# Kernel tuning notes

Hardware: AMD Instinct MI355X
Metric: run time of the kernel (lower is better)

## Reference

```python
import jax, jax.numpy as jnp
import numpy as np

B, V, M, H, L, T = 4, 2048, 8192, 64, 5, 4


def setup_inputs() -> dict:
    key = jax.random.key(0)
    ks = jax.random.split(key, 24)
    inp = {
        "input_llr": jax.random.normal(ks[0], (B, V), jnp.float32),
        "message_to_var_mapping": jax.random.randint(ks[1], (M,), 0, V, jnp.int32),
        "message_types": jax.random.randint(ks[2], (M,), 0, T, jnp.int32),
        "var_to_check_adjacency": jax.random.uniform(ks[3], (M, M), jnp.float32),
        "check_to_var_adjacency": jax.random.uniform(ks[4], (M, M), jnp.float32),
    }
    s = 0.05
    # input_embedding: Linear(1, H)
    inp["w_in"] = jax.random.normal(ks[5], (H,), jnp.float32) * s
    inp["b_in"] = jax.random.normal(ks[6], (H,), jnp.float32) * s
    # per-layer params, stacked over L iterations
    inp["type_emb"] = jax.random.normal(ks[7], (L, T, H), jnp.float32) * s
    inp["w1v"] = jax.random.normal(ks[8], (L, 2 * H, H), jnp.float32) * s
    inp["b1v"] = jax.random.normal(ks[9], (L, H), jnp.float32) * s
    inp["w2v"] = jax.random.normal(ks[10], (L, H, H), jnp.float32) * s
    inp["b2v"] = jax.random.normal(ks[11], (L, H), jnp.float32) * s
    inp["w1c"] = jax.random.normal(ks[12], (L, 2 * H, H), jnp.float32) * s
    inp["b1c"] = jax.random.normal(ks[13], (L, H), jnp.float32) * s
    inp["w2c"] = jax.random.normal(ks[14], (L, H, H), jnp.float32) * s
    inp["b2c"] = jax.random.normal(ks[15], (L, H), jnp.float32) * s
    # output_projection of the LAST gnn layer (the one used by decode_messages)
    inp["proj_w"] = jax.random.normal(ks[16], (H,), jnp.float32) * s
    inp["proj_b"] = jax.random.normal(ks[17], (), jnp.float32) * s
    return inp


def reference(input_llr, message_to_var_mapping, message_types,
              var_to_check_adjacency, check_to_var_adjacency,
              w_in, b_in, type_emb, w1v, b1v, w2v, b2v,
              w1c, b1c, w2c, b2c, proj_w, proj_b):
    Bv, Vn = input_llr.shape
    # gather message LLRs from variable nodes: (B, M)
    msg_llr = input_llr[:, message_to_var_mapping]
    # input embedding Linear(1, H): (B, M, H)
    feat = msg_llr[..., None] * w_in + b_in
    safe_types = jnp.clip(message_types, 0, T - 1)
    n_layers = type_emb.shape[0]
    for i in range(n_layers):
        te = type_emb[i][safe_types]                      # (M, H)
        comb = feat + te                                  # (B, M, H)
        v2c = jnp.einsum('mn,bnh->bmh', var_to_check_adjacency, comb)
        uv = jnp.concatenate([comb, v2c], axis=-1)        # (B, M, 2H)
        uv = jax.nn.relu(uv @ w1v[i] + b1v[i]) @ w2v[i] + b2v[i]
        c2v = jnp.einsum('mn,bnh->bmh', check_to_var_adjacency, comb)
        uc = jnp.concatenate([comb, c2v], axis=-1)
        uc = jax.nn.relu(uc @ w1c[i] + b1c[i]) @ w2c[i] + b2c[i]
        upd = uv + uc
        if i > 0:  # residual applied only after first iteration (per source)
            upd = upd + feat
        feat = upd
    # decode with last layer's output projection: (B, M)
    decoded = feat @ proj_w + proj_b
    # sum-aggregate message LLRs back to variable nodes: (B, V)
    var_llrs = jax.ops.segment_sum(decoded.T, message_to_var_mapping,
                                   num_segments=Vn).T
    return jax.nn.sigmoid(var_llrs + input_llr)
```

## Files before the change

kernel.cpp:

```cpp
#include <hip/hip_runtime.h>
#include <math.h>

static constexpr int CB = 4;
static constexpr int CV = 2048;
static constexpr int CM = 8192;
static constexpr int CH = 64;
static constexpr int CL = 5;
static constexpr int CT = 4;
static constexpr int RR = CM * CB;
static constexpr int WCAT_STRIDE = 192 * 128 + 128 * 64 + 128 + 64;
static constexpr size_t SLAB = (size_t)CM * 256;

typedef float f32x4 __attribute__((ext_vector_type(4)));
typedef short bf16x8 __attribute__((ext_vector_type(8)));
typedef unsigned int u32;
typedef unsigned short u16;

__device__ inline u16 f2bf(float x) {
    u32 u = __float_as_uint(x);
    u += 0x7FFF + ((u >> 16) & 1);
    return (u16)(u >> 16);
}
__device__ inline float bf2f(u16 b) { return __uint_as_float(((u32)b) << 16); }

#define GLOAD16(gp, lp)                                                         \
    __builtin_amdgcn_global_load_lds(                                           \
        (const __attribute__((address_space(1))) unsigned int*)(gp),            \
        (__attribute__((address_space(3))) unsigned int*)(lp), 16, 0, 0)

__global__ void k_init_feat(const float* __restrict__ llr, const int* __restrict__ map,
                            const float* __restrict__ w_in, const float* __restrict__ b_in,
                            float* __restrict__ feat) {
    int idx = blockIdx.x * blockDim.x + threadIdx.x;
    int h = idx & 63;
    int r = idx >> 6;
    int m = r >> 2;
    int b = r & 3;
    float v = llr[b * CV + map[m]];
    feat[idx] = v * w_in[h] + b_in[h];
}

__global__ void k_comb(const float* __restrict__ feat, const int* __restrict__ types,
                       const float* __restrict__ te, float* __restrict__ in2) {
    int idx = blockIdx.x * blockDim.x + threadIdx.x;
    int h = idx & 63;
    int r = idx >> 6;
    int m = r >> 2;
    int t = types[m];
    t = t < 0 ? 0 : (t > CT - 1 ? CT - 1 : t);
    in2[(size_t)r * 192 + h] = feat[idx] + te[t * CH + h];
}

__global__ __launch_bounds__(256) void k_splitA(const float* __restrict__ Avc,
                                                const float* __restrict__ Acv,
                                                u16* __restrict__ Aprep) {
    __shared__ float lds[16][548];
    const int blk = blockIdx.x;
    const int adj = blk >> 13;
    const int rem = blk & 8191;
    const int rf = rem & 511;
    const int kig = rem >> 9;
    const float* __restrict__ A = adj ? Acv : Avc;
    const int t = threadIdx.x;
    {
        const int rl = t >> 4, cc = t & 15;
        const float* rp = A + (size_t)(rf * 16 + rl) * CM + kig * 512 + cc * 32;
        const int cbase = cc * 32 + ((cc & 7) << 2);
#pragma unroll
        for (int j = 0; j < 8; ++j) {
            float4 v = *(const float4*)(rp + j * 4);
            *(float4*)&lds[rl][cbase + j * 4] = v;
        }
    }
    __syncthreads();
    {
        const int lane = t & 63, w = t >> 6;
        const int r = lane & 15, c = lane >> 4;
#pragma unroll
        for (int i = 0; i < 4; ++i) {
            const int kl = w * 4 + i;
            const int cbase = kl * 32 + ((kl & 7) << 2) + c * 8;
            float4 v0 = *(const float4*)&lds[r][cbase];
            float4 v1 = *(const float4*)&lds[r][cbase + 4];
            float e[8] = {v0.x, v0.y, v0.z, v0.w, v1.x, v1.y, v1.z, v1.w};
            u32 hw[4], lw[4];
#pragma unroll
            for (int j = 0; j < 4; ++j) {
                float a0 = e[2 * j], a1 = e[2 * j + 1];
                u16 h0 = f2bf(a0), h1 = f2bf(a1);
                u16 g0 = f2bf(a0 - bf2f(h0)), g1 = f2bf(a1 - bf2f(h1));
                hw[j] = (u32)h0 | ((u32)h1 << 16);
                lw[j] = (u32)g0 | ((u32)g1 << 16);
            }
            u16* dp = Aprep + (((size_t)adj * 256 + kig * 16 + kl) * 512 + rf) * 1024
                    + (size_t)lane * 8;
            *(uint4*)dp = make_uint4(hw[0], hw[1], hw[2], hw[3]);
            *(uint4*)(dp + 512) = make_uint4(lw[0], lw[1], lw[2], lw[3]);
        }
    }
}

__global__ void k_transposeB(const float* __restrict__ feat, const int* __restrict__ types,
                             const float* __restrict__ te, char* __restrict__ BprepC,
                             float* __restrict__ comb) {
    __shared__ float tile[64][65];
    __shared__ float teL[4][64];
    __shared__ int ty[64];
    const int tid = threadIdx.x;
    const int m0 = blockIdx.x * 64;
    teL[tid >> 6][tid & 63] = te[tid];
    if (tid < 64) {
        int tt = types[m0 + tid];
        ty[tid] = tt < 0 ? 0 : (tt > CT - 1 ? CT - 1 : tt);
    }
    __syncthreads();
    for (int b = 0; b < 4; ++b) {
        __syncthreads();
        {
            const int mr = tid >> 2, hc = (tid & 3) * 16;
            const float* fp = feat + ((size_t)(m0 + mr) * 4 + b) * 64 + hc;
            float* op = comb + ((size_t)(m0 + mr) * 4 + b) * 64 + hc;
            const int tt = ty[mr];
#pragma unroll
            for (int j = 0; j < 4; ++j) {
                float4 v = *(const float4*)(fp + j * 4);
                float4 c;
                c.x = v.x + teL[tt][hc + j * 4 + 0];
                c.y = v.y + teL[tt][hc + j * 4 + 1];
                c.z = v.z + teL[tt][hc + j * 4 + 2];
                c.w = v.w + teL[tt][hc + j * 4 + 3];
                tile[mr][hc + j * 4 + 0] = c.x;
                tile[mr][hc + j * 4 + 1] = c.y;
                tile[mr][hc + j * 4 + 2] = c.z;
                tile[mr][hc + j * 4 + 3] = c.w;
                *(float4*)(op + j * 4) = c;
            }
        }
        __syncthreads();
        {
            const int h = tid & 63, mg = tid >> 6;
            u32 hw[8], lw[8];
#pragma unroll
            for (int q = 0; q < 8; ++q) {
                float v0 = tile[mg * 16 + 2 * q + 0][h];
                float v1 = tile[mg * 16 + 2 * q + 1][h];
                u16 h0 = f2bf(v0), h1 = f2bf(v1);
                u16 g0 = f2bf(v0 - bf2f(h0)), g1 = f2bf(v1 - bf2f(h1));
                hw[q] = (u32)h0 | ((u32)h1 << 16);
                lw[q] = (u32)g0 | ((u32)g1 << 16);
            }
            const int c = b * 64 + h;
            const int mstart = m0 + mg * 16;
            const int ki = mstart >> 5;
            const int q0 = (mstart >> 3) & 3;
            const int swzc = (c & 7) << 4;
            char* rowp = BprepC + (size_t)ki * 32768 + c * 128;
            *(uint4*)(rowp + (((q0 + 0) * 16) ^ swzc)) = make_uint4(hw[0], hw[1], hw[2], hw[3]);
            *(uint4*)(rowp + (((q0 + 1) * 16) ^ swzc)) = make_uint4(hw[4], hw[5], hw[6], hw[7]);
            *(uint4*)(rowp + (((4 + q0) * 16) ^ swzc)) = make_uint4(lw[0], lw[1], lw[2], lw[3]);
            *(uint4*)(rowp + (((5 + q0) * 16) ^ swzc)) = make_uint4(lw[4], lw[5], lw[6], lw[7]);
        }
    }
}

__global__ __launch_bounds__(512, 1) void k_adjmfma_fast(
    const char* __restrict__ AprepC, const char* __restrict__ BprepC,
    float* __restrict__ pbuf) {
    __shared__ char frames[3][49152];

    int lin = blockIdx.y * 64 + blockIdx.x;
    lin = (lin & 7) * 32 + (lin >> 3);
    const int bx = lin & 63;
    const int by = lin >> 6;
    const int adj = by >> 1;
    const int ks = by & 1;

    const int tid = threadIdx.x;
    const int lane = tid & 63;
    const int wid = tid >> 6;
    const int wr = wid >> 2;
    const int wc = wid & 3;
    const int l15 = lane & 15, l4 = lane >> 4;
    const int m0 = bx * 128;

    const size_t abase = (((size_t)adj * 256) * 512 + (size_t)bx * 8) * 2048;

#define STAGE3(FP, S)                                                            \
    {                                                                            \
        int ki_ = ks * 128 + (S); if (ki_ > 255) ki_ = 255;                      \
        const char* as_ = AprepC + abase + (size_t)ki_ * (512 * 2048);           \
        GLOAD16(as_ + tid * 16, (FP) + tid * 16);                                \
        GLOAD16(as_ + 8192 + tid * 16, (FP) + 8192 + tid * 16);                  \
        const char* bs_ = BprepC + ((size_t)ki_ << 15);                          \
        GLOAD16(bs_ + tid * 16, (FP) + 16384 + tid * 16);                        \
        GLOAD16(bs_ + 8192 + tid * 16, (FP) + 24576 + tid * 16);                 \
        GLOAD16(bs_ + 16384 + tid * 16, (FP) + 32768 + tid * 16);                \
        GLOAD16(bs_ + 24576 + tid * 16, (FP) + 40960 + tid * 16);                \
    }

    f32x4 acc[4][4] = {};

    STAGE3(&frames[0][0], 0);
    STAGE3(&frames[1][0], 1);
    STAGE3(&frames[2][0], 2);

    int f = 0;
    for (int s = 0; s < 128; ++s) {
        asm volatile("s_waitcnt vmcnt(12)" ::: "memory");
        asm volatile("s_barrier" ::: "memory");
        const char* fr = &frames[f][0];
        bf16x8 bh[4], bl[4];
#pragma unroll
        for (int nf = 0; nf < 4; ++nf) {
            const int col = wc * 64 + nf * 16 + l15;
            const char* rb = fr + 16384 + col * 128;
            const int swz = (col & 7) << 4;
            bh[nf] = *(const bf16x8*)(rb + ((l4 * 16) ^ swz));
            bl[nf] = *(const bf16x8*)(rb + (((4 + l4) * 16) ^ swz));
        }
#pragma unroll
        for (int mf = 0; mf < 4; ++mf) {
            const char* ra = fr + (wr * 4 + mf) * 2048 + lane * 16;
            bf16x8 ah = *(const bf16x8*)ra;
            bf16x8 al = *(const bf16x8*)(ra + 1024);
#pragma unroll
            for (int nf = 0; nf < 4; ++nf) {
                acc[mf][nf] = __builtin_amdgcn_mfma_f32_16x16x32_bf16(ah, bh[nf], acc[mf][nf], 0, 0, 0);
                acc[mf][nf] = __builtin_amdgcn_mfma_f32_16x16x32_bf16(ah, bl[nf], acc[mf][nf], 0, 0, 0);
                acc[mf][nf] = __builtin_amdgcn_mfma_f32_16x16x32_bf16(al, bh[nf], acc[mf][nf], 0, 0, 0);
            }
        }
        asm volatile("s_barrier" ::: "memory");
        STAGE3(fr, s + 3);
        f = (f == 2) ? 0 : f + 1;
    }
    asm volatile("s_waitcnt vmcnt(0)" ::: "memory");

    float* pb = pbuf + (size_t)by * SLAB;
#pragma unroll
    for (int mf = 0; mf < 4; ++mf) {
#pragma unroll
        for (int nf = 0; nf < 4; ++nf) {
            const int col = wc * 64 + nf * 16 + l15;
#pragma unroll
            for (int r = 0; r < 4; ++r) {
                const int m = m0 + wr * 64 + mf * 16 + l4 * 4 + r;
                pb[(size_t)m * 256 + col] = acc[mf][nf][r];
            }
        }
    }
#undef STAGE3
}

__global__ __launch_bounds__(256) void k_gemm1f(
    const float* __restrict__ comb, const float* __restrict__ pbuf,
    const float* __restrict__ wc, float* __restrict__ hid) {
    __shared__ float As[32][64];
    __shared__ float Bs[32][68];

    const int tid = threadIdx.x;
    const int m0 = blockIdx.y * 64;
    const int c0 = blockIdx.x * 64;
    const int tm = (tid & 15) * 4;
    const int tn = (tid >> 4) * 4;
    const int arow = tid & 63;
    const int akg = (tid >> 6) * 8;
    const int bk = tid >> 4;
    const int bc = (tid & 15) * 4;
    const float* bias = wc + 32768;

    float acc[4][4] = {};

    for (int k0 = 0; k0 < 192; k0 += 32) {
        const int krow = k0 + akg;
        const int r = m0 + arow;
        float4 a0, a1;
        if (krow < 64) {
            const float* ap = comb + (size_t)r * 64 + krow;
            a0 = *(const float4*)ap;
            a1 = *(const float4*)(ap + 4);
        } else {
            const int adj = (krow - 64) >> 6;
            const int h = (krow - 64) & 63;
            const float* p = pbuf + (size_t)(adj * 2) * SLAB
                           + (size_t)(r >> 2) * 256 + (r & 3) * 64 + h;
            float4 x0 = *(const float4*)p;
            float4 x1 = *(const float4*)(p + 4);
            float4 y0 = *(const float4*)(p + SLAB);
            float4 y1 = *(const float4*)(p + SLAB + 4);
            a0.x = x0.x + y0.x; a0.y = x0.y + y0.y; a0.z = x0.z + y0.z; a0.w = x0.w + y0.w;
            a1.x = x1.x + y1.x; a1.y = x1.y + y1.y; a1.z = x1.z + y1.z; a1.w = x1.w + y1.w;
        }
        float4 b0 = *(const float4*)(wc + (size_t)(k0 + bk) * 128 + c0 + bc);
        float4 b1 = *(const float4*)(wc + (size_t)(k0 + bk + 16) * 128 + c0 + bc);
        As[akg + 0][arow] = a0.x;
        As[akg + 1][arow] = a0.y;
        As[akg + 2][arow] = a0.z;
        As[akg + 3][arow] = a0.w;
        As[akg + 4][arow] = a1.x;
        As[akg + 5][arow] = a1.y;
        As[akg + 6][arow] = a1.z;
        As[akg + 7][arow] = a1.w;
        *(float4*)&Bs[bk][bc] = b0;
        *(float4*)&Bs[bk + 16][bc] = b1;
        __syncthreads();
#pragma unroll
        for (int k = 0; k < 32; ++k) {
            float4 av = *(const float4*)&As[k][tm];
            float4 bv = *(const float4*)&Bs[k][tn];
            float a_[4] = {av.x, av.y, av.z, av.w};
            float b_[4] = {bv.x, bv.y, bv.z, bv.w};
#pragma unroll
            for (int i = 0; i < 4; ++i)
#pragma unroll
                for (int j = 0; j < 4; ++j)
                    acc[i][j] = fmaf(a_[i], b_[j], acc[i][j]);
        }
        __syncthreads();
    }

#pragma unroll
    for (int i = 0; i < 4; ++i) {
        int m = m0 + tm + i;
        float4 x = make_float4(acc[i][0], acc[i][1], acc[i][2], acc[i][3]);
        const float4 bv = *(const float4*)&bias[c0 + tn];
        x.x = fmaxf(x.x + bv.x, 0.f);
        x.y = fmaxf(x.y + bv.y, 0.f);
        x.z = fmaxf(x.z + bv.z, 0.f);
        x.w = fmaxf(x.w + bv.w, 0.f);
        *(float4*)&hid[(size_t)m * 128 + c0 + tn] = x;
    }
}

__global__ void k_transpose(const float* __restrict__ feat, const int* __restrict__ types,
                            const float* __restrict__ te,
                            u16* __restrict__ BH, u16* __restrict__ BL) {
    __shared__ float tile[64][65];
    __shared__ float teL[4][64];
    __shared__ int ty[64];
    const int tid = threadIdx.x;
    const int m0 = blockIdx.x * 64;
    teL[tid >> 6][tid & 63] = te[tid];
    if (tid < 64) {
        int t = types[m0 + tid];
        ty[tid] = t < 0 ? 0 : (t > CT - 1 ? CT - 1 : t);
    }
    __syncthreads();
    for (int b = 0; b < 4; ++b) {
        __syncthreads();
        {
            const int mr = tid >> 2, hc = (tid & 3) * 16;
            const float* fp = feat + ((size_t)(m0 + mr) * 4 + b) * 64 + hc;
            const int t = ty[mr];
#pragma unroll
            for (int j = 0; j < 4; ++j) {
                float4 v = *(const float4*)(fp + j * 4);
                tile[mr][hc + j * 4 + 0] = v.x + teL[t][hc + j * 4 + 0];
                tile[mr][hc + j * 4 + 1] = v.y + teL[t][hc + j * 4 + 1];
                tile[mr][hc + j * 4 + 2] = v.z + teL[t][hc + j * 4 + 2];
                tile[mr][hc + j * 4 + 3] = v.w + teL[t][hc + j * 4 + 3];
            }
        }
        __syncthreads();
        {
            const int h = tid & 63, mg = tid >> 6;
            u32 hw[8], lw[8];
#pragma unroll
            for (int q = 0; q < 8; ++q) {
                float v0 = tile[mg * 16 + 2 * q + 0][h];
                float v1 = tile[mg * 16 + 2 * q + 1][h];
                u16 h0 = f2bf(v0), h1 = f2bf(v1);
                u16 g0 = f2bf(v0 - bf2f(h0)), g1 = f2bf(v1 - bf2f(h1));
                hw[q] = (u32)h0 | ((u32)h1 << 16);
                lw[q] = (u32)g0 | ((u32)g1 << 16);
            }
            size_t obase = (size_t)(b * 64 + h) * CM + m0 + mg * 16;
            *(uint4*)(BH + obase) = make_uint4(hw[0], hw[1], hw[2], hw[3]);
            *(uint4*)(BH + obase + 8) = make_uint4(hw[4], hw[5], hw[6], hw[7]);
            *(uint4*)(BL + obase) = make_uint4(lw[0], lw[1], lw[2], lw[3]);
            *(uint4*)(BL + obase + 8) = make_uint4(lw[4], lw[5], lw[6], lw[7]);
        }
    }
}

__global__ __launch_bounds__(512, 2) void k_adjmfma_fb(
    const float* __restrict__ A0, const float* __restrict__ A1,
    const u16* __restrict__ BH, const u16* __restrict__ BL,
    float* __restrict__ pbuf) {
    __shared__ char lA[128 * 128];
    __shared__ char lB[256 * 128];

    const int tid = threadIdx.x;
    const int adj = blockIdx.y >> 1;
    const int ks = blockIdx.y & 1;
    const int m0 = blockIdx.x * 128;
    const float* __restrict__ A = adj ? A1 : A0;
    const int kbase = ks * 4096;

    const int lane = tid & 63;
    const int wid = tid >> 6;
    const int wr = wid >> 2;
    const int wc = wid & 3;
    const int l15 = lane & 15, l4 = lane >> 4;

    const int sa_row = tid >> 2, sa_kq = tid & 3;
    const int sb_col = tid >> 1, sb_part = tid & 1;

    f32x4 acc[4][4] = {};

    for (int k0 = 0; k0 < 4096; k0 += 32) {
        {
            const float* ap = A + (size_t)(m0 + sa_row) * CM + kbase + k0 + sa_kq * 8;
            float4 v0 = *(const float4*)ap;
            float4 v1 = *(const float4*)(ap + 4);
            float vv[8] = {v0.x, v0.y, v0.z, v0.w, v1.x, v1.y, v1.z, v1.w};
            u32 hw[4], lw[4];
#pragma unroll
            for (int j = 0; j < 4; ++j) {
                float a0 = vv[2 * j], a1 = vv[2 * j + 1];
                u16 h0 = f2bf(a0), h1 = f2bf(a1);
                u16 g0 = f2bf(a0 - bf2f(h0)), g1 = f2bf(a1 - bf2f(h1));
                hw[j] = (u32)h0 | ((u32)h1 << 16);
                lw[j] = (u32)g0 | ((u32)g1 << 16);
            }
            char* base = lA + sa_row * 128;
            const int swz = (sa_row & 7) << 4;
            *(uint4*)(base + ((sa_kq * 16) ^ swz)) = make_uint4(hw[0], hw[1], hw[2], hw[3]);
            *(uint4*)(base + ((64 + sa_kq * 16) ^ swz)) = make_uint4(lw[0], lw[1], lw[2], lw[3]);
        }
        {
            const u16* src = (sb_part ? BL : BH) + (size_t)sb_col * CM + kbase + k0;
            char* base = lB + sb_col * 128;
            const int swz = (sb_col & 7) << 4;
            const int lb = sb_part * 64;
#pragma unroll
            for (int j = 0; j < 4; ++j) {
                uint4 v = *(const uint4*)(src + j * 8);
                *(uint4*)(base + ((lb + j * 16) ^ swz)) = v;
            }
        }
        __syncthreads();

        bf16x8 bh[4], bl[4];
#pragma unroll
        for (int nf = 0; nf < 4; ++nf) {
            const int col = wc * 64 + nf * 16 + l15;
            const char* rb = lB + col * 128;
            const int swz = (col & 7) << 4;
            bh[nf] = *(const bf16x8*)(rb + ((l4 * 16) ^ swz));
            bl[nf] = *(const bf16x8*)(rb + ((64 + l4 * 16) ^ swz));
        }
#pragma unroll
        for (int mf = 0; mf < 4; ++mf) {
            const int row = wr * 64 + mf * 16 + l15;
            const char* ra = lA + row * 128;
            const int swz = (row & 7) << 4;
            bf16x8 ah = *(const bf16x8*)(ra + ((l4 * 16) ^ swz));
            bf16x8 al = *(const bf16x8*)(ra + ((64 + l4 * 16) ^ swz));
#pragma unroll
            for (int nf = 0; nf < 4; ++nf) {
                acc[mf][nf] = __builtin_amdgcn_mfma_f32_16x16x32_bf16(ah, bh[nf], acc[mf][nf], 0, 0, 0);
                acc[mf][nf] = __builtin_amdgcn_mfma_f32_16x16x32_bf16(ah, bl[nf], acc[mf][nf], 0, 0, 0);
                acc[mf][nf] = __builtin_amdgcn_mfma_f32_16x16x32_bf16(al, bh[nf], acc[mf][nf], 0, 0, 0);
            }
        }
        __syncthreads();
    }

    float* pb = pbuf + (size_t)blockIdx.y * SLAB;
#pragma unroll
    for (int mf = 0; mf < 4; ++mf) {
#pragma unroll
        for (int nf = 0; nf < 4; ++nf) {
            const int col = wc * 64 + nf * 16 + l15;
#pragma unroll
            for (int r = 0; r < 4; ++r) {
                const int m = m0 + wr * 64 + mf * 16 + l4 * 4 + r;
                pb[(size_t)m * 256 + col] = acc[mf][nf][r];
            }
        }
    }
}

__global__ void k_reduce(const float* __restrict__ pbuf, float* __restrict__ in2) {
    int idx = blockIdx.x * blockDim.x + threadIdx.x;
    int adj = idx >> 19;
    int rem = idx & ((1 << 19) - 1);
    int m = rem >> 6;
    int f4 = rem & 63;
    size_t o = (size_t)m * 256 + (size_t)f4 * 4;
    const float* p0 = pbuf + (size_t)(adj * 2) * SLAB;
    const float* p1 = p0 + SLAB;
    float4 a = *(const float4*)(p0 + o);
    float4 b4 = *(const float4*)(p1 + o);
    a.x += b4.x; a.y += b4.y; a.z += b4.z; a.w += b4.w;
    int col = f4 * 4;
    int bb = col >> 6, h = col & 63;
    *(float4*)&in2[((size_t)m * 4 + bb) * 192 + 64 + adj * 64 + h] = a;
}

__global__ void k_prep(const float* __restrict__ w1v, const float* __restrict__ b1v,
                       const float* __restrict__ w2v, const float* __restrict__ b2v,
                       const float* __restrict__ w1c, const float* __restrict__ b1c,
                       const float* __restrict__ w2c, const float* __restrict__ b2c,
                       float* __restrict__ wcat) {
    int idx = blockIdx.x * blockDim.x + threadIdx.x;
    int total = CL * WCAT_STRIDE;
    if (idx >= total) return;
    int i = idx / WCAT_STRIDE;
    int e = idx % WCAT_STRIDE;
    float v;
    if (e < 24576) {
        int j = e >> 7, k = e & 127;
        if (j < 64)        v = (k < 64) ? w1v[(i * 128 + j) * 64 + k]
                                        : w1c[(i * 128 + j) * 64 + (k - 64)];
        else if (j < 128)  v = (k < 64) ? w1v[(i * 128 + j) * 64 + k] : 0.f;
        else               v = (k < 64) ? 0.f : w1c[(i * 128 + (j - 64)) * 64 + (k - 64)];
    } else if (e < 32768) {
        int e2 = e - 24576; int k = e2 >> 6, h = e2 & 63;
        v = (k < 64) ? w2v[(i * 64 + k) * 64 + h]
                     : w2c[(i * 64 + (k - 64)) * 64 + h];
    } else if (e < 32896) {
        int k = e - 32768;
        v = (k < 64) ? b1v[i * 64 + k] : b1c[i * 64 + (k - 64)];
    } else {
        int h = e - 32896;
        v = b2v[i * 64 + h] + b2c[i * 64 + h];
    }
    wcat[idx] = v;
}

template<int OMODE, int RES>
__global__ __launch_bounds__(256) void k_gemm(
    const float* __restrict__ A0, int lda,
    const float* __restrict__ Bm, int ldb,
    float* __restrict__ O, const float* __restrict__ bias,
    const float* __restrict__ resid, int K) {
    __shared__ float As[32][64];
    __shared__ float Bs[32][68];

    const int tid = threadIdx.x;
    const int m0 = blockIdx.y * 64;
    const int c0 = blockIdx.x * 64;
    const int tm = (tid & 15) * 4;
    const int tn = (tid >> 4) * 4;
    const int arow = tid & 63;
    const int akg = (tid >> 6) * 8;
    const int bk = tid >> 4;
    const int bc = (tid & 15) * 4;

    float acc[4][4] = {};

    for (int k0 = 0; k0 < K; k0 += 32) {
        const float* Ap = A0 + (size_t)(m0 + arow) * (size_t)lda + k0 + akg;
        float4 a0 = *(const float4*)Ap;
        float4 a1 = *(const float4*)(Ap + 4);
        float4 b0 = *(const float4*)(Bm + (size_t)(k0 + bk) * (size_t)ldb + c0 + bc);
        float4 b1 = *(const float4*)(Bm + (size_t)(k0 + bk + 16) * (size_t)ldb + c0 + bc);
        As[akg + 0][arow] = a0.x;
        As[akg + 1][arow] = a0.y;
        As[akg + 2][arow] = a0.z;
        As[akg + 3][arow] = a0.w;
        As[akg + 4][arow] = a1.x;
        As[akg + 5][arow] = a1.y;
        As[akg + 6][arow] = a1.z;
        As[akg + 7][arow] = a1.w;
        *(float4*)&Bs[bk][bc] = b0;
        *(float4*)&Bs[bk + 16][bc] = b1;
        __syncthreads();
#pragma unroll
        for (int k = 0; k < 32; ++k) {
            float4 av = *(const float4*)&As[k][tm];
            float4 bv = *(const float4*)&Bs[k][tn];
            float a_[4] = {av.x, av.y, av.z, av.w};
            float b_[4] = {bv.x, bv.y, bv.z, bv.w};
#pragma unroll
            for (int i = 0; i < 4; ++i)
#pragma unroll
                for (int j = 0; j < 4; ++j)
                    acc[i][j] = fmaf(a_[i], b_[j], acc[i][j]);
        }
        __syncthreads();
    }

#pragma unroll
    for (int i = 0; i < 4; ++i) {
        int m = m0 + tm + i;
        float4 x = make_float4(acc[i][0], acc[i][1], acc[i][2], acc[i][3]);
        if (OMODE == 1) {
            const float4 bv = *(const float4*)&bias[c0 + tn];
            x.x = fmaxf(x.x + bv.x, 0.f);
            x.y = fmaxf(x.y + bv.y, 0.f);
            x.z = fmaxf(x.z + bv.z, 0.f);
            x.w = fmaxf(x.w + bv.w, 0.f);
            *(float4*)&O[(size_t)m * 128 + c0 + tn] = x;
        } else {
            const float4 bv = *(const float4*)&bias[tn];
            x.x += bv.x; x.y += bv.y; x.z += bv.z; x.w += bv.w;
            if (RES) {
                const float4 rv = *(const float4*)&resid[(size_t)m * 64 + tn];
                x.x += rv.x; x.y += rv.y; x.z += rv.z; x.w += rv.w;
            }
            *(float4*)&O[(size_t)m * 64 + tn] = x;
        }
    }
}

__global__ void k_zero(float* __restrict__ p, int n) {
    int i = blockIdx.x * blockDim.x + threadIdx.x;
    if (i < n) p[i] = 0.f;
}

__global__ void k_decode(const float* __restrict__ feat, const float* __restrict__ proj_w,
                         const float* __restrict__ proj_b, const int* __restrict__ map,
                         float* __restrict__ var_llrs) {
    int r = blockIdx.x * 4 + (threadIdx.x >> 6);
    int lane = threadIdx.x & 63;
    float v = feat[(size_t)r * 64 + lane] * proj_w[lane];
#pragma unroll
    for (int off = 32; off > 0; off >>= 1) v += __shfl_down(v, off);
    if (lane == 0) {
        int m = r >> 2, b = r & 3;
        atomicAdd(&var_llrs[b * CV + map[m]], v + proj_b[0]);
    }
}

__global__ void k_final(const float* __restrict__ var_llrs, const float* __restrict__ llr,
                        float* __restrict__ out) {
    int i = blockIdx.x * blockDim.x + threadIdx.x;
    float x = var_llrs[i] + llr[i];
    out[i] = 1.f / (1.f + expf(-x));
}

extern "C" void kernel_launch(void* const* d_in, const int* in_sizes, int n_in,
                              void* d_out, int out_size, void* d_ws, size_t ws_size,
                              hipStream_t stream) {
    const float* llr   = (const float*)d_in[0];
    const int*   map   = (const int*)d_in[1];
    const int*   types = (const int*)d_in[2];
    const float* Avc   = (const float*)d_in[3];
    const float* Acv   = (const float*)d_in[4];
    const float* w_in  = (const float*)d_in[5];
    const float* b_in  = (const float*)d_in[6];
    const float* temb  = (const float*)d_in[7];
    const float* w1v   = (const float*)d_in[8];
    const float* b1v   = (const float*)d_in[9];
    const float* w2v   = (const float*)d_in[10];
    const float* b2v   = (const float*)d_in[11];
    const float* w1c   = (const float*)d_in[12];
    const float* b1c   = (const float*)d_in[13];
    const float* w2c   = (const float*)d_in[14];
    const float* b2c   = (const float*)d_in[15];
    const float* projw = (const float*)d_in[16];
    const float* projb = (const float*)d_in[17];
    float* out = (float*)d_out;

    constexpr size_t OFF_FEAT = 0;
    constexpr size_t OFF_IN2  = OFF_FEAT + (size_t)RR * 64 * 4;
    constexpr size_t OFF_HID  = OFF_IN2 + (size_t)RR * 192 * 4;
    constexpr size_t OFF_WCAT = OFF_HID + (size_t)RR * 128 * 4;
    constexpr size_t OFF_VLLR = OFF_WCAT + (size_t)CL * WCAT_STRIDE * 4;
    constexpr size_t OFF_PBUF = OFF_VLLR + 8192 * 4;
    constexpr size_t OFF_X    = OFF_PBUF + (size_t)4 * SLAB * 4;
    constexpr size_t BPREP_BYTES = (size_t)256 * 32768 + 32768;
    constexpr size_t OFF_APREP   = OFF_X + BPREP_BYTES;
    constexpr size_t APREP_BYTES = (size_t)2 * 256 * 512 * 2048 + 8192;
    constexpr size_t NEED_FAST   = OFF_APREP + APREP_BYTES;
    constexpr size_t OFF_CTH = OFF_X;
    constexpr size_t OFF_CTL = OFF_CTH + (size_t)256 * CM * 2;

    char* ws = (char*)d_ws;
    float* feat = (float*)(ws + OFF_FEAT);
    float* in2  = (float*)(ws + OFF_IN2);
    float* comb = (float*)(ws + OFF_IN2);
    float* hid  = (float*)(ws + OFF_HID);
    float* wcat = (float*)(ws + OFF_WCAT);
    float* vllr = (float*)(ws + OFF_VLLR);
    float* pbuf = (float*)(ws + OFF_PBUF);
    char* Bprep = ws + OFF_X;
    u16* combTH = (u16*)(ws + OFF_CTH);
    u16* combTL = (u16*)(ws + OFF_CTL);
    u16* Aprep  = (u16*)(ws + OFF_APREP);

    const bool fast = ws_size >= NEED_FAST;

    k_zero<<<(CB * CV + 255) / 256, 256, 0, stream>>>(vllr, CB * CV);
    k_prep<<<(CL * WCAT_STRIDE + 255) / 256, 256, 0, stream>>>(
        w1v, b1v, w2v, b2v, w1c, b1c, w2c, b2c, wcat);
    k_init_feat<<<(RR * CH) / 256, 256, 0, stream>>>(llr, map, w_in, b_in, feat);

    if (fast)
        k_splitA<<<16384, 256, 0, stream>>>(Avc, Acv, Aprep);

    for (int i = 0; i < CL; ++i) {
        float* wc = wcat + (size_t)i * WCAT_STRIDE;
        const float* te = temb + i * CT * CH;
        if (fast) {
            k_transposeB<<<CM / 64, 256, 0, stream>>>(feat, types, te, Bprep, comb);
            k_adjmfma_fast<<<dim3(64, 4), 512, 0, stream>>>(
                (const char*)Aprep, Bprep, pbuf);
            k_gemm1f<<<dim3(2, 512), 256, 0, stream>>>(comb, pbuf, wc, hid);
        } else {
            k_comb<<<(RR * CH) / 256, 256, 0, stream>>>(feat, types, te, in2);
            k_transpose<<<CM / 64, 256, 0, stream>>>(feat, types, te, combTH, combTL);
            k_adjmfma_fb<<<dim3(64, 4), 512, 0, stream>>>(Avc, Acv, combTH, combTL, pbuf);
            k_reduce<<<(2 * CM * 64) / 256, 256, 0, stream>>>(pbuf, in2);
            k_gemm<1, 0><<<dim3(2, 512), 256, 0, stream>>>(
                in2, 192, wc, 128, hid, wc + 32768, nullptr, 192);
        }
        if (i == 0)
            k_gemm<2, 0><<<dim3(1, 512), 256, 0, stream>>>(
                hid, 128, wc + 24576, 64, feat, wc + 32896, feat, 128);
        else
            k_gemm<2, 1><<<dim3(1, 512), 256, 0, stream>>>(
                hid, 128, wc + 24576, 64, feat, wc + 32896, feat, 128);
    }

    k_decode<<<RR / 4, 256, 0, stream>>>(feat, projw, projb, map, vllr);
    k_final<<<(CB * CV) / 256, 256, 0, stream>>>(vllr, llr, out);
}
```

Baseline: 1.354 ms.

## Load B operand directly into registers in MFMA fragment layout, shrinking LDS frames

```diff
diff --git a/kernel.cpp b/kernel.cpp
--- a/kernel.cpp
+++ b/kernel.cpp
@@ -101,7 +101,7 @@
 }
 
 __global__ void k_transposeB(const float* __restrict__ feat, const int* __restrict__ types,
-                             const float* __restrict__ te, char* __restrict__ BprepC,
+                             const float* __restrict__ te, char* __restrict__ Bprep2,
                              float* __restrict__ comb) {
     __shared__ float tile[64][65];
     __shared__ float teL[4][64];
@@ -150,23 +150,28 @@
                 lw[q] = (u32)g0 | ((u32)g1 << 16);
             }
             const int c = b * 64 + h;
+            const int l15c = c & 15;
+            const int nfc = (c >> 4) & 3;
             const int mstart = m0 + mg * 16;
             const int ki = mstart >> 5;
-            const int q0 = (mstart >> 3) & 3;
-            const int swzc = (c & 7) << 4;
-            char* rowp = BprepC + (size_t)ki * 32768 + c * 128;
-            *(uint4*)(rowp + (((q0 + 0) * 16) ^ swzc)) = make_uint4(hw[0], hw[1], hw[2], hw[3]);
-            *(uint4*)(rowp + (((q0 + 1) * 16) ^ swzc)) = make_uint4(hw[4], hw[5], hw[6], hw[7]);
-            *(uint4*)(rowp + (((4 + q0) * 16) ^ swzc)) = make_uint4(lw[0], lw[1], lw[2], lw[3]);
-            *(uint4*)(rowp + (((5 + q0) * 16) ^ swzc)) = make_uint4(lw[4], lw[5], lw[6], lw[7]);
+            const int koff0 = mstart & 31;
+            u32* bp = (u32*)Bprep2 + (size_t)(ki * 4 + b) * 2048;
+#pragma unroll
+            for (int q = 0; q < 8; ++q) {
+                const int koff = koff0 + 2 * q;
+                const int lane = (koff >> 3) * 16 + l15c;
+                const int jq = (koff & 7) >> 1;
+                bp[(size_t)lane * 32 + nfc * 4 + jq] = hw[q];
+                bp[(size_t)lane * 32 + (4 + nfc) * 4 + jq] = lw[q];
+            }
         }
     }
 }
 
 __global__ __launch_bounds__(512, 1) void k_adjmfma_fast(
-    const char* __restrict__ AprepC, const char* __restrict__ BprepC,
+    const char* __restrict__ AprepC, const char* __restrict__ Bprep2,
     float* __restrict__ pbuf) {
-    __shared__ char frames[3][49152];
+    __shared__ char frames[3][16384];
 
     int lin = blockIdx.y * 64 + blockIdx.x;
     lin = (lin & 7) * 32 + (lin >> 3);
@@ -183,56 +188,73 @@
     const int l15 = lane & 15, l4 = lane >> 4;
     const int m0 = bx * 128;
 
-    const size_t abase = (((size_t)adj * 256) * 512 + (size_t)bx * 8) * 2048;
-
-#define STAGE3(FP, S)                                                            \
+    const size_t abase = (((size_t)adj * 256 + ks * 128) * 512 + (size_t)bx * 8) * 2048;
+    const char* bwave = Bprep2 + (size_t)wc * 8192 + (size_t)lane * 128;
+
+#define ASTAGE(FR, S)                                                            \
     {                                                                            \
-        int ki_ = ks * 128 + (S); if (ki_ > 255) ki_ = 255;                      \
-        const char* as_ = AprepC + abase + (size_t)ki_ * (512 * 2048);           \
-        GLOAD16(as_ + tid * 16, (FP) + tid * 16);                                \
-        GLOAD16(as_ + 8192 + tid * 16, (FP) + 8192 + tid * 16);                  \
-        const char* bs_ = BprepC + ((size_t)ki_ << 15);                          \
-        GLOAD16(bs_ + tid * 16, (FP) + 16384 + tid * 16);                        \
-        GLOAD16(bs_ + 8192 + tid * 16, (FP) + 24576 + tid * 16);                 \
-        GLOAD16(bs_ + 16384 + tid * 16, (FP) + 32768 + tid * 16);                \
-        GLOAD16(bs_ + 24576 + tid * 16, (FP) + 40960 + tid * 16);                \
+        int s_ = (S) > 127 ? 127 : (S);                                          \
+        const char* as_ = AprepC + abase + (size_t)s_ * (512 * 2048);            \
+        GLOAD16(as_ + tid * 16, (FR) + tid * 16);                                \
+        GLOAD16(as_ + 8192 + tid * 16, (FR) + 8192 + tid * 16);                  \
+    }
+#define BLOAD(BHr, BLr, S)                                                       \
+    {                                                                            \
+        int s_ = (S) > 127 ? 127 : (S);                                          \
+        const char* bp_ = bwave + ((size_t)(ks * 128 + s_) << 15);               \
+        _Pragma("unroll")                                                        \
+        for (int nf = 0; nf < 4; ++nf) {                                         \
+            BHr[nf] = *(const bf16x8*)(bp_ + nf * 16);                           \
+            BLr[nf] = *(const bf16x8*)(bp_ + 64 + nf * 16);                      \
+        }                                                                        \
+    }
+#define COMPUTE(FR, BHr, BLr)                                                    \
+    {                                                                            \
+        _Pragma("unroll")                                                        \
+        for (int mf = 0; mf < 4; ++mf) {                                         \
+            const char* ra = (FR) + (wr * 4 + mf) * 2048 + lane * 16;            \
+            bf16x8 ah = *(const bf16x8*)ra;                                      \
+            bf16x8 al = *(const bf16x8*)(ra + 1024);                             \
+            _Pragma("unroll")                                                    \
+            for (int nf = 0; nf < 4; ++nf) {                                     \
+                acc[mf][nf] = __builtin_amdgcn_mfma_f32_16x16x32_bf16(ah, BHr[nf], acc[mf][nf], 0, 0, 0); \
+                acc[mf][nf] = __builtin_amdgcn_mfma_f32_16x16x32_bf16(ah, BLr[nf], acc[mf][nf], 0, 0, 0); \
+                acc[mf][nf] = __builtin_amdgcn_mfma_f32_16x16x32_bf16(al, BHr[nf], acc[mf][nf], 0, 0, 0); \
+            }                                                                    \
+        }                                                                        \
     }
 
     f32x4 acc[4][4] = {};
-
-    STAGE3(&frames[0][0], 0);
-    STAGE3(&frames[1][0], 1);
-    STAGE3(&frames[2][0], 2);
+    bf16x8 bh0[4], bl0[4], bh1[4], bl1[4];
+
+    ASTAGE(&frames[0][0], 0);
+    BLOAD(bh0, bl0, 0);
+    ASTAGE(&frames[1][0], 1);
+    BLOAD(bh1, bl1, 1);
+    ASTAGE(&frames[2][0], 2);
 
     int f = 0;
-    for (int s = 0; s < 128; ++s) {
-        asm volatile("s_waitcnt vmcnt(12)" ::: "memory");
-        asm volatile("s_barrier" ::: "memory");
-        const char* fr = &frames[f][0];
-        bf16x8 bh[4], bl[4];
-#pragma unroll
-        for (int nf = 0; nf < 4; ++nf) {
-            const int col = wc * 64 + nf * 16 + l15;
-            const char* rb = fr + 16384 + col * 128;
-            const int swz = (col & 7) << 4;
-            bh[nf] = *(const bf16x8*)(rb + ((l4 * 16) ^ swz));
-            bl[nf] = *(const bf16x8*)(rb + (((4 + l4) * 16) ^ swz));
-        }
-#pragma unroll
-        for (int mf = 0; mf < 4; ++mf) {
-            const char* ra = fr + (wr * 4 + mf) * 2048 + lane * 16;
-            bf16x8 ah = *(const bf16x8*)ra;
-            bf16x8 al = *(const bf16x8*)(ra + 1024);
-#pragma unroll
-            for (int nf = 0; nf < 4; ++nf) {
-                acc[mf][nf] = __builtin_amdgcn_mfma_f32_16x16x32_bf16(ah, bh[nf], acc[mf][nf], 0, 0, 0);
-                acc[mf][nf] = __builtin_amdgcn_mfma_f32_16x16x32_bf16(ah, bl[nf], acc[mf][nf], 0, 0, 0);
-                acc[mf][nf] = __builtin_amdgcn_mfma_f32_16x16x32_bf16(al, bh[nf], acc[mf][nf], 0, 0, 0);
-            }
-        }
-        asm volatile("s_barrier" ::: "memory");
-        STAGE3(fr, s + 3);
-        f = (f == 2) ? 0 : f + 1;
+    for (int ss = 0; ss < 128; ss += 2) {
+        {
+            asm volatile("s_waitcnt vmcnt(12)" ::: "memory");
+            asm volatile("s_barrier" ::: "memory");
+            const char* fr = &frames[f][0];
+            COMPUTE(fr, bh0, bl0);
+            BLOAD(bh0, bl0, ss + 2);
+            asm volatile("s_barrier" ::: "memory");
+            ASTAGE(&frames[f][0], ss + 3);
+            f = (f == 2) ? 0 : f + 1;
+        }
+        {
+            asm volatile("s_waitcnt vmcnt(12)" ::: "memory");
+            asm volatile("s_barrier" ::: "memory");
+            const char* fr = &frames[f][0];
+            COMPUTE(fr, bh1, bl1);
+            BLOAD(bh1, bl1, ss + 3);
+            asm volatile("s_barrier" ::: "memory");
+            ASTAGE(&frames[f][0], ss + 4);
+            f = (f == 2) ? 0 : f + 1;
+        }
     }
     asm volatile("s_waitcnt vmcnt(0)" ::: "memory");
 
@@ -249,7 +271,9 @@
             }
         }
     }
-#undef STAGE3
+#undef ASTAGE
+#undef BLOAD
+#undef COMPUTE
 }
 
 __global__ __launch_bounds__(256) void k_gemm1f(
@@ -677,7 +701,7 @@
     float* wcat = (float*)(ws + OFF_WCAT);
     float* vllr = (float*)(ws + OFF_VLLR);
     float* pbuf = (float*)(ws + OFF_PBUF);
-    char* Bprep = ws + OFF_X;
+    char* Bprep2 = ws + OFF_X;
     u16* combTH = (u16*)(ws + OFF_CTH);
     u16* combTL = (u16*)(ws + OFF_CTL);
     u16* Aprep  = (u16*)(ws + OFF_APREP);
@@ -696,9 +720,9 @@
         float* wc = wcat + (size_t)i * WCAT_STRIDE;
         const float* te = temb + i * CT * CH;
         if (fast) {
-            k_transposeB<<<CM / 64, 256, 0, stream>>>(feat, types, te, Bprep, comb);
+            k_transposeB<<<CM / 64, 256, 0, stream>>>(feat, types, te, Bprep2, comb);
             k_adjmfma_fast<<<dim3(64, 4), 512, 0, stream>>>(
-                (const char*)Aprep, Bprep, pbuf);
+                (const char*)Aprep, Bprep2, pbuf);
             k_gemm1f<<<dim3(2, 512), 256, 0, stream>>>(comb, pbuf, wc, hid);
         } else {
             k_comb<<<(RR * CH) / 256, 256, 0, stream>>>(feat, types, te, in2);
```

Result: slower. 2.156 ms (+59.2%).
